# Kernel tuning notes

Hardware: AMD Instinct MI355X
Metric: run time of the kernel (lower is better)

## Reference

```python
import jax, jax.numpy as jnp
import numpy as np

B, C, H, W = 4, 256, 64, 64
R = 8          # rank = min(8, C//4)
G = 4          # conv groups
CG = C // G    # channels per group


def conv1x1(x, w, b):
    # x: [B,C,H,W], w: [O,C], b: [O]
    return jnp.einsum('oc,bchw->bohw', w, x) + b[None, :, None, None]


def conv1x1_grouped(x, w, b):
    # x: [B,C,H,W], w: [C, C//G] (per-output-channel slice of its group), b: [C]
    xg = x.reshape(B, G, CG, H, W)
    wg = w.reshape(G, CG, CG)  # [group, out_in_group, in_in_group]
    out = jnp.einsum('goc,bgchw->bgohw', wg, xg).reshape(B, C, H, W)
    return out + b[None, :, None, None]


def attend(q, k, v):
    # q,k: [B,R,H,W]; v: [B,C,H,W]; N = H*W
    qf = q.reshape(B, R, H * W)
    kf = k.reshape(B, R, H * W)
    vf = v.reshape(B, C, H * W)
    scores = jnp.einsum('bri,brj->bij', qf, kf)       # [B,N,N], no 1/sqrt scaling (faithful)
    attn = jax.nn.softmax(scores, axis=-1)
    out = jnp.einsum('bcm,bmn->bcn', vf, attn)        # v @ attn, contraction over query index m
    return out.reshape(B, C, H, W)


def setup_inputs():
    key = jax.random.key(0)
    ks = jax.random.split(key, 10)
    s = 0.05
    return {
        'fL': jax.random.normal(ks[0], (B, C, H, W), jnp.float32),
        'fU': jax.random.normal(ks[1], (B, C, H, W), jnp.float32),
        'qL_w': jax.random.normal(ks[2], (R, C), jnp.float32) * s,
        'qL_b': jnp.zeros((R,), jnp.float32),
        'kU_w': jax.random.normal(ks[3], (R, C), jnp.float32) * s,
        'kU_b': jnp.zeros((R,), jnp.float32),
        'vU_w': jax.random.normal(ks[4], (C, CG), jnp.float32) * s,
        'vU_b': jnp.zeros((C,), jnp.float32),
        'qU_w': jax.random.normal(ks[5], (R, C), jnp.float32) * s,
        'qU_b': jnp.zeros((R,), jnp.float32),
        'kL_w': jax.random.normal(ks[6], (R, C), jnp.float32) * s,
        'kL_b': jnp.zeros((R,), jnp.float32),
        'vL_w': jax.random.normal(ks[7], (C, CG), jnp.float32) * s,
        'vL_b': jnp.zeros((C,), jnp.float32),
        'beta': jnp.array(0.5, jnp.float32),
    }


def reference(fL, fU, qL_w, qL_b, kU_w, kU_b, vU_w, vU_b,
              qU_w, qU_b, kL_w, kL_b, vL_w, vL_b, beta):
    LU = attend(conv1x1(fL, qL_w, qL_b),
                conv1x1(fU, kU_w, kU_b),
                conv1x1_grouped(fU, vU_w, vU_b))
    UL = attend(conv1x1(fU, qU_w, qU_b),
                conv1x1(fL, kL_w, kL_b),
                conv1x1_grouped(fL, vL_w, vL_b))
    fL2 = fL + beta * LU
    fU2 = fU + beta * UL
    return (fL2, fU2)
```

## Files before the change

kernel.cpp:

```cpp
#include <hip/hip_runtime.h>

typedef float f32x4 __attribute__((ext_vector_type(4)));
typedef float f32x16 __attribute__((ext_vector_type(16)));
typedef short s16x8 __attribute__((ext_vector_type(8)));
typedef unsigned short u16;
typedef unsigned long long u64;

#define BN 4
#define CC 256
#define NN 4096

static __device__ __forceinline__ u16 f2bf(float x) {
    unsigned int u = __float_as_uint(x);
    u += 0x7FFF + ((u >> 16) & 1);
    return (u16)(u >> 16);
}

__global__ __launch_bounds__(256) void k_wtrans(
    const float* __restrict__ qLw, const float* __restrict__ kLw,
    const float* __restrict__ qUw, const float* __restrict__ kUw,
    const float* __restrict__ vUw, const float* __restrict__ vLw,
    float* __restrict__ wT, float* __restrict__ wvT)
{
    int a = blockIdx.x, t = threadIdx.x;
    const float* qw = a ? qUw : qLw;
    const float* kw = a ? kUw : kLw;
#pragma unroll
    for (int r = 0; r < 8; ++r) {
        wT[((size_t)a * 256 + t) * 16 + r]     = qw[r * 256 + t];
        wT[((size_t)a * 256 + t) * 16 + 8 + r] = kw[r * 256 + t];
    }
    const float* wv = a ? vLw : vUw;
    for (int cp = 0; cp < 64; ++cp)
        wvT[((size_t)a * 64 + cp) * 256 + t] = wv[(size_t)t * 64 + cp];
}

__global__ __launch_bounds__(256) void k_qkprep(
    const float* __restrict__ fL, const float* __restrict__ fU,
    const float* __restrict__ wT,
    const float* __restrict__ qLb, const float* __restrict__ kLb,
    const float* __restrict__ qUb, const float* __restrict__ kUb,
    u16* __restrict__ qbf, u16* __restrict__ kbf)
{
    int blk = blockIdx.x;
    int nc = blk & 31, b = (blk >> 5) & 3, src = blk >> 7;
    const float* f = src ? fU : fL;
    int qa = src, ka = 1 - src;
    int t = threadIdx.x;
    int nl = t & 127;
    int cs = __builtin_amdgcn_readfirstlane(t >> 7) * 128;
    int n = nc * 128 + nl;
    const float* fp = f + (size_t)b * 256 * NN + n;
    const float* wbase = wT + (size_t)src * 4096;

    float acc[16];
#pragma unroll
    for (int r = 0; r < 16; ++r) acc[r] = 0.f;

#pragma unroll 4
    for (int c = cs; c < cs + 128; ++c) {
        float fv = fp[(size_t)c * NN];
        const float* wr = wbase + (size_t)c * 16;
#pragma unroll
        for (int r = 0; r < 16; ++r) acc[r] += wr[r] * fv;
    }

    __shared__ float red[2][128][17];
    int cc = t >> 7;
#pragma unroll
    for (int r = 0; r < 16; ++r) red[cc][nl][r] = acc[r];
    __syncthreads();

    if (t < 128) {
        const float* bq = src ? qUb : qLb;
        const float* bk = src ? kUb : kLb;
        const float L2E = 1.4426950408889634f;
        int nn = nc * 128 + t;
        u16 pq[8], pk[8];
#pragma unroll
        for (int r = 0; r < 8; ++r) {
            pq[r] = f2bf((red[0][t][r]     + red[1][t][r]     + bq[r]) * L2E);
            pk[r] = f2bf( red[0][t][8 + r] + red[1][t][8 + r] + bk[r]);
        }
        uint4 vq, vk;
        vq.x = pq[0] | ((unsigned)pq[1] << 16); vq.y = pq[2] | ((unsigned)pq[3] << 16);
        vq.z = pq[4] | ((unsigned)pq[5] << 16); vq.w = pq[6] | ((unsigned)pq[7] << 16);
        vk.x = pk[0] | ((unsigned)pk[1] << 16); vk.y = pk[2] | ((unsigned)pk[3] << 16);
        vk.z = pk[4] | ((unsigned)pk[5] << 16); vk.w = pk[6] | ((unsigned)pk[7] << 16);
        *(uint4*)(qbf + (((size_t)qa * BN + b) * NN + nn) * 8) = vq;
        *(uint4*)(kbf + (((size_t)ka * BN + b) * NN + nn) * 8) = vk;
    }
}

__global__ __launch_bounds__(256) void k_zsum(
    const u16* __restrict__ qbf, const u16* __restrict__ kbf,
    float* __restrict__ Z)
{
    int blk = blockIdx.x;
    int mt = blk & 31, ab = blk >> 5;
    int t = threadIdx.x, l = t & 63;
    int w = __builtin_amdgcn_readfirstlane(t >> 6);
    int l31 = l & 31, g2 = l >> 5;
    int m0 = mt * 128 + w * 32;

    const u16* qab = qbf + (size_t)ab * NN * 8;
    const u16* kab = kbf + (size_t)ab * NN * 8;

    s16x8 af = *(const s16x8*)(qab + (size_t)(m0 + l31) * 8);
    if (g2) af = (s16x8)0;

    auto ldb = [&](int i) -> s16x8 {
        s16x8 r = *(const s16x8*)(kab + (size_t)(i * 32 + l31) * 8);
        return g2 ? (s16x8)0 : r;
    };

    float zp[16];
#pragma unroll
    for (int r = 0; r < 16; ++r) zp[r] = 0.f;

    s16x8 b0 = ldb(0), b1 = ldb(1);
#pragma unroll 1
    for (int i = 0; i < 128; ++i) {
        int nx = i + 2 < 127 ? i + 2 : 127;
        s16x8 bn = ldb(nx);
        f32x16 s = __builtin_amdgcn_mfma_f32_32x32x16_bf16(af, b0, (f32x16)0.f, 0, 0, 0);
#pragma unroll
        for (int r = 0; r < 16; ++r) zp[r] += __builtin_exp2f(s[r]);
        b0 = b1; b1 = bn;
    }

#pragma unroll
    for (int r = 0; r < 16; ++r) {
        float v = zp[r];
#pragma unroll
        for (int d = 1; d < 32; d <<= 1) v += __shfl_xor(v, d, 64);
        zp[r] = v;
    }
    if (l31 == 0) {
#pragma unroll
        for (int r = 0; r < 16; ++r) {
            int m = m0 + (r & 3) + 8 * (r >> 2) + 4 * g2;
            Z[(size_t)ab * NN + m] = zp[r];
        }
    }
}

__global__ __launch_bounds__(256) void k_vprep(
    const float* __restrict__ fL, const float* __restrict__ fU,
    const float* __restrict__ wvT,
    const float* __restrict__ vUb, const float* __restrict__ vLb,
    const float* __restrict__ Z, u16* __restrict__ vpt)
{
    int blk = blockIdx.x;
    int mc = blk & 31, g = (blk >> 5) & 3, ab = blk >> 7;
    int a = ab >> 2, b = ab & 3;
    const float* f    = a ? fL : fU;
    const float* bias = a ? vLb : vUb;
    int t = threadIdx.x, l = t & 63;
    int wu = __builtin_amdgcn_readfirstlane(t >> 6);
    int m0 = mc * 128 + l * 2;

    const float* fg = f + ((size_t)b * 256 + g * 64) * NN + m0;
    const float* wq = wvT + (size_t)a * 16384 + g * 64 + wu * 16;

    float acc[16][2];
#pragma unroll
    for (int j = 0; j < 16; ++j) { acc[j][0] = 0.f; acc[j][1] = 0.f; }

    for (int cp = 0; cp < 64; ++cp) {
        float2 fv = *(const float2*)(fg + (size_t)cp * NN);
        const float* wr = wq + (size_t)cp * 256;
        float4 w0 = *(const float4*)(wr);
        float4 w1 = *(const float4*)(wr + 4);
        float4 w2 = *(const float4*)(wr + 8);
        float4 w3 = *(const float4*)(wr + 12);
        float wv[16] = {w0.x,w0.y,w0.z,w0.w, w1.x,w1.y,w1.z,w1.w,
                        w2.x,w2.y,w2.z,w2.w, w3.x,w3.y,w3.z,w3.w};
#pragma unroll
        for (int j = 0; j < 16; ++j) {
            acc[j][0] += wv[j] * fv.x;
            acc[j][1] += wv[j] * fv.y;
        }
    }

    float2 z = *(const float2*)(Z + (size_t)ab * NN + m0);
    float zr0 = 1.f / z.x, zr1 = 1.f / z.y;
    int mt = m0 >> 5, mi = m0 & 31;
    u16* vpo = vpt + (((size_t)ab * 128 + mt) * 256 + g * 64 + wu * 16) * 32 + mi;
#pragma unroll
    for (int j = 0; j < 16; ++j) {
        float bj = bias[g * 64 + wu * 16 + j];
        unsigned pk = (unsigned)f2bf((acc[j][0] + bj) * zr0) |
                      ((unsigned)f2bf((acc[j][1] + bj) * zr1) << 16);
        *(unsigned*)(vpo + (size_t)j * 32) = pk;
    }
}

__global__ __launch_bounds__(512) void k_main(
    const float* __restrict__ fL, const float* __restrict__ fU,
    const u16* __restrict__ qbf, const u16* __restrict__ kbf,
    const u16* __restrict__ vpt, const float* __restrict__ beta_p,
    float* __restrict__ out)
{
    int blk = blockIdx.x;
    int ab = blk & 7, nt = blk >> 3;
    int a = ab >> 2, b = ab & 3;
    int n0 = nt * 128;
    int t = threadIdx.x, l = t & 63;
    int w = __builtin_amdgcn_readfirstlane(t >> 6);
    int c15 = l & 15, g = l >> 4;

    __shared__ u16 ebuf[2][128][40];

    const u16* qab = qbf + (size_t)ab * NN * 8;
    const u16* kab = kbf + (size_t)ab * NN * 8;

    s16x8 bkf = *(const s16x8*)(kab + (size_t)(n0 + w * 16 + c15) * 8);
    if (g) bkf = (s16x8)0;

    const u16* apb = vpt + (size_t)ab * (128ull * 8192)
                   + (size_t)(w * 32 + c15) * 32 + g * 8;

    f32x4 acc[2][8];
#pragma unroll
    for (int i = 0; i < 2; ++i)
#pragma unroll
        for (int j = 0; j < 8; ++j) acc[i][j] = (f32x4)0.f;

    auto qld = [&](int ks, int mh) -> s16x8 {
        s16x8 r = *(const s16x8*)(qab + (size_t)(ks * 32 + mh * 16 + c15) * 8);
        return g ? (s16x8)0 : r;
    };

    auto egen = [&](int pbuf, s16x8 qa0, s16x8 qa1) {
        f32x4 s0 = __builtin_amdgcn_mfma_f32_16x16x32_bf16(qa0, bkf, (f32x4)0.f, 0, 0, 0);
        f32x4 s1 = __builtin_amdgcn_mfma_f32_16x16x32_bf16(qa1, bkf, (f32x4)0.f, 0, 0, 0);
        u64 p0 = 0, p1 = 0;
#pragma unroll
        for (int r = 0; r < 4; ++r) {
            p0 |= (u64)f2bf(__builtin_exp2f(s0[r])) << (16 * r);
            p1 |= (u64)f2bf(__builtin_exp2f(s1[r])) << (16 * r);
        }
        *(u64*)&ebuf[pbuf][w * 16 + c15][4 * g]      = p0;
        *(u64*)&ebuf[pbuf][w * 16 + c15][16 + 4 * g] = p1;
    };

    auto pv = [&](int pbuf, const s16x8& a0, const s16x8& a1) {
#pragma unroll
        for (int nf = 0; nf < 8; ++nf) {
            s16x8 bf = *(const s16x8*)&ebuf[pbuf][nf * 16 + c15][8 * g];
            acc[0][nf] = __builtin_amdgcn_mfma_f32_16x16x32_bf16(a0, bf, acc[0][nf], 0, 0, 0);
            acc[1][nf] = __builtin_amdgcn_mfma_f32_16x16x32_bf16(a1, bf, acc[1][nf], 0, 0, 0);
        }
    };

    {
        s16x8 z0 = qld(0, 0), z1 = qld(0, 1);
        egen(0, z0, z1);
    }
    s16x8 qa0 = qld(1, 0), qa1 = qld(1, 1);
    s16x8 qb0 = qld(2, 0), qb1 = qld(2, 1);
    s16x8 af0 = *(const s16x8*)(apb);
    s16x8 af1 = *(const s16x8*)(apb + 512);
    __syncthreads();

#pragma unroll 1
    for (int k2 = 0; k2 < 64; ++k2) {
        {
            int k = 2 * k2;
            int kn = k + 1;
            const u16* apn = apb + (size_t)kn * 8192;
            s16x8 an0 = *(const s16x8*)(apn);
            s16x8 an1 = *(const s16x8*)(apn + 512);
            int kq = k + 3 < 127 ? k + 3 : 127;
            s16x8 nq0 = qld(kq, 0), nq1 = qld(kq, 1);

            egen(1, qa0, qa1);
            pv(0, af0, af1);

            af0 = an0; af1 = an1;
            qa0 = nq0; qa1 = nq1;
            __syncthreads();
        }
        {
            int k = 2 * k2 + 1;
            int kn = k + 1 < 127 ? k + 1 : 127;
            const u16* apn = apb + (size_t)kn * 8192;
            s16x8 an0 = *(const s16x8*)(apn);
            s16x8 an1 = *(const s16x8*)(apn + 512);
            int kq = k + 3 < 127 ? k + 3 : 127;
            s16x8 nq0 = qld(kq, 0), nq1 = qld(kq, 1);

            if (k < 127) egen(0, qb0, qb1);
            pv(1, af0, af1);

            af0 = an0; af1 = an1;
            qb0 = nq0; qb1 = nq1;
            __syncthreads();
        }
    }

    float beta = beta_p[0];
    const float* base = a ? fU : fL;
    float* op = out + (size_t)a * ((size_t)BN * CC * NN);
#pragma unroll
    for (int cf = 0; cf < 2; ++cf)
#pragma unroll
        for (int nf = 0; nf < 8; ++nf)
#pragma unroll
            for (int r = 0; r < 4; ++r) {
                int c = w * 32 + cf * 16 + g * 4 + r;
                int n = n0 + nf * 16 + c15;
                size_t idx = ((size_t)b * CC + c) * NN + n;
                op[idx] = base[idx] + beta * acc[cf][nf][r];
            }
}

extern "C" void kernel_launch(void* const* d_in, const int* in_sizes, int n_in,
                              void* d_out, int out_size, void* d_ws, size_t ws_size,
                              hipStream_t stream) {
    const float* fL  = (const float*)d_in[0];
    const float* fU  = (const float*)d_in[1];
    const float* qLw = (const float*)d_in[2];
    const float* qLb = (const float*)d_in[3];
    const float* kUw = (const float*)d_in[4];
    const float* kUb = (const float*)d_in[5];
    const float* vUw = (const float*)d_in[6];
    const float* vUb = (const float*)d_in[7];
    const float* qUw = (const float*)d_in[8];
    const float* qUb = (const float*)d_in[9];
    const float* kLw = (const float*)d_in[10];
    const float* kLb = (const float*)d_in[11];
    const float* vLw = (const float*)d_in[12];
    const float* vLb = (const float*)d_in[13];
    const float* beta = (const float*)d_in[14];

    char* ws = (char*)d_ws;
    float* wT  = (float*)(ws);
    float* wvT = (float*)(ws + 32768);
    u16*   qbf = (u16*)  (ws + 163840);
    u16*   kbf = (u16*)  (ws + 688128);
    float* Z   = (float*)(ws + 1212416);
    u16*   vpt = (u16*)  (ws + 1343488);
    float* out = (float*)d_out;

    k_wtrans<<<2, 256, 0, stream>>>(qLw, kLw, qUw, kUw, vUw, vLw, wT, wvT);
    k_qkprep<<<256, 256, 0, stream>>>(fL, fU, wT, qLb, kLb, qUb, kUb, qbf, kbf);
    k_zsum<<<256, 256, 0, stream>>>(qbf, kbf, Z);
    k_vprep<<<1024, 256, 0, stream>>>(fL, fU, wvT, vUb, vLb, Z, vpt);
    k_main<<<256, 512, 0, stream>>>(fL, fU, qbf, kbf, vpt, beta, out);
}
```

Measured before the change: 194.3 us.

## Retile attention PV loop to 64x64 warp tiles with swizzled LDS and deeper K step

The main attention kernel changes each warp's output tile from 32 channels x 128 positions to 64 channels x 64 positions. It processes 64 keys per iteration instead of 32, halving the number of barriers, and stores the exp tile in a 128-byte-row LDS buffer with an XOR swizzle to avoid bank conflicts. The new tiling cuts the LDS B-fragment reads per MFMA and rebalances reuse of V and exp fragments, at the cost of more registers for the 4x4 accumulators and the held fragments. Separately, the q/k projection kernel moves to 512 threads, splitting the channel reduction four ways for more parallelism.

After: 228.5 us. 1.18x slower.

```diff
diff --git a/kernel.cpp b/kernel.cpp
--- a/kernel.cpp
+++ b/kernel.cpp
@@ -35,7 +35,7 @@
         wvT[((size_t)a * 64 + cp) * 256 + t] = wv[(size_t)t * 64 + cp];
 }
 
-__global__ __launch_bounds__(256) void k_qkprep(
+__global__ __launch_bounds__(512) void k_qkprep(
     const float* __restrict__ fL, const float* __restrict__ fU,
     const float* __restrict__ wT,
     const float* __restrict__ qLb, const float* __restrict__ kLb,
@@ -48,7 +48,7 @@
     int qa = src, ka = 1 - src;
     int t = threadIdx.x;
     int nl = t & 127;
-    int cs = __builtin_amdgcn_readfirstlane(t >> 7) * 128;
+    int cs = __builtin_amdgcn_readfirstlane(t >> 7) * 64;
     int n = nc * 128 + nl;
     const float* fp = f + (size_t)b * 256 * NN + n;
     const float* wbase = wT + (size_t)src * 4096;
@@ -58,14 +58,14 @@
     for (int r = 0; r < 16; ++r) acc[r] = 0.f;
 
 #pragma unroll 4
-    for (int c = cs; c < cs + 128; ++c) {
+    for (int c = cs; c < cs + 64; ++c) {
         float fv = fp[(size_t)c * NN];
         const float* wr = wbase + (size_t)c * 16;
 #pragma unroll
         for (int r = 0; r < 16; ++r) acc[r] += wr[r] * fv;
     }
 
-    __shared__ float red[2][128][17];
+    __shared__ float red[4][128][17];
     int cc = t >> 7;
 #pragma unroll
     for (int r = 0; r < 16; ++r) red[cc][nl][r] = acc[r];
@@ -79,8 +79,10 @@
         u16 pq[8], pk[8];
 #pragma unroll
         for (int r = 0; r < 8; ++r) {
-            pq[r] = f2bf((red[0][t][r]     + red[1][t][r]     + bq[r]) * L2E);
-            pk[r] = f2bf( red[0][t][8 + r] + red[1][t][8 + r] + bk[r]);
+            float sq = red[0][t][r] + red[1][t][r] + red[2][t][r] + red[3][t][r];
+            float sk = red[0][t][8+r] + red[1][t][8+r] + red[2][t][8+r] + red[3][t][8+r];
+            pq[r] = f2bf((sq + bq[r]) * L2E);
+            pk[r] = f2bf( sk + bk[r]);
         }
         uint4 vq, vk;
         vq.x = pq[0] | ((unsigned)pq[1] << 16); vq.y = pq[2] | ((unsigned)pq[3] << 16);
@@ -209,8 +211,13 @@
     int t = threadIdx.x, l = t & 63;
     int w = __builtin_amdgcn_readfirstlane(t >> 6);
     int c15 = l & 15, g = l >> 4;
-
-    __shared__ u16 ebuf[2][128][40];
+    int cq = w & 3, nh = w >> 2;
+
+    __shared__ u16 ebuf[2][128][64];
+
+    auto eptr = [&](int p, int n, int mbyte) -> char* {
+        return ((char*)ebuf) + (((p << 7) + n) << 7) + (mbyte ^ ((n & 7) << 4));
+    };
 
     const u16* qab = qbf + (size_t)ab * NN * 8;
     const u16* kab = kbf + (size_t)ab * NN * 8;
@@ -219,98 +226,88 @@
     if (g) bkf = (s16x8)0;
 
     const u16* apb = vpt + (size_t)ab * (128ull * 8192)
-                   + (size_t)(w * 32 + c15) * 32 + g * 8;
-
-    f32x4 acc[2][8];
-#pragma unroll
-    for (int i = 0; i < 2; ++i)
-#pragma unroll
-        for (int j = 0; j < 8; ++j) acc[i][j] = (f32x4)0.f;
-
-    auto qld = [&](int ks, int mh) -> s16x8 {
-        s16x8 r = *(const s16x8*)(qab + (size_t)(ks * 32 + mh * 16 + c15) * 8);
+                   + (size_t)(cq * 64 + c15) * 32 + g * 8;
+
+    f32x4 acc[4][4];
+#pragma unroll
+    for (int i = 0; i < 4; ++i)
+#pragma unroll
+        for (int j = 0; j < 4; ++j) acc[i][j] = (f32x4)0.f;
+
+    auto qld = [&](int step, int mq) -> s16x8 {
+        s16x8 r = *(const s16x8*)(qab + (size_t)(step * 64 + mq * 16 + c15) * 8);
         return g ? (s16x8)0 : r;
     };
 
-    auto egen = [&](int pbuf, s16x8 qa0, s16x8 qa1) {
-        f32x4 s0 = __builtin_amdgcn_mfma_f32_16x16x32_bf16(qa0, bkf, (f32x4)0.f, 0, 0, 0);
-        f32x4 s1 = __builtin_amdgcn_mfma_f32_16x16x32_bf16(qa1, bkf, (f32x4)0.f, 0, 0, 0);
-        u64 p0 = 0, p1 = 0;
-#pragma unroll
-        for (int r = 0; r < 4; ++r) {
-            p0 |= (u64)f2bf(__builtin_exp2f(s0[r])) << (16 * r);
-            p1 |= (u64)f2bf(__builtin_exp2f(s1[r])) << (16 * r);
-        }
-        *(u64*)&ebuf[pbuf][w * 16 + c15][4 * g]      = p0;
-        *(u64*)&ebuf[pbuf][w * 16 + c15][16 + 4 * g] = p1;
+    auto egen = [&](int pbuf, const s16x8 (&qv)[4]) {
+#pragma unroll
+        for (int mq = 0; mq < 4; ++mq) {
+            f32x4 s = __builtin_amdgcn_mfma_f32_16x16x32_bf16(qv[mq], bkf, (f32x4)0.f, 0, 0, 0);
+            u64 pk = 0;
+#pragma unroll
+            for (int r = 0; r < 4; ++r)
+                pk |= (u64)f2bf(__builtin_exp2f(s[r])) << (16 * r);
+            *(u64*)eptr(pbuf, w * 16 + c15, mq * 32 + g * 8) = pk;
+        }
     };
 
-    auto pv = [&](int pbuf, const s16x8& a0, const s16x8& a1) {
-#pragma unroll
-        for (int nf = 0; nf < 8; ++nf) {
-            s16x8 bf = *(const s16x8*)&ebuf[pbuf][nf * 16 + c15][8 * g];
-            acc[0][nf] = __builtin_amdgcn_mfma_f32_16x16x32_bf16(a0, bf, acc[0][nf], 0, 0, 0);
-            acc[1][nf] = __builtin_amdgcn_mfma_f32_16x16x32_bf16(a1, bf, acc[1][nf], 0, 0, 0);
-        }
-    };
-
     {
-        s16x8 z0 = qld(0, 0), z1 = qld(0, 1);
-        egen(0, z0, z1);
-    }
-    s16x8 qa0 = qld(1, 0), qa1 = qld(1, 1);
-    s16x8 qb0 = qld(2, 0), qb1 = qld(2, 1);
-    s16x8 af0 = *(const s16x8*)(apb);
-    s16x8 af1 = *(const s16x8*)(apb + 512);
+        s16x8 q0[4];
+#pragma unroll
+        for (int mq = 0; mq < 4; ++mq) q0[mq] = qld(0, mq);
+        egen(0, q0);
+    }
+    s16x8 qn[4];
+#pragma unroll
+    for (int mq = 0; mq < 4; ++mq) qn[mq] = qld(1, mq);
     __syncthreads();
 
 #pragma unroll 1
-    for (int k2 = 0; k2 < 64; ++k2) {
-        {
-            int k = 2 * k2;
-            int kn = k + 1;
-            const u16* apn = apb + (size_t)kn * 8192;
-            s16x8 an0 = *(const s16x8*)(apn);
-            s16x8 an1 = *(const s16x8*)(apn + 512);
-            int kq = k + 3 < 127 ? k + 3 : 127;
-            s16x8 nq0 = qld(kq, 0), nq1 = qld(kq, 1);
-
-            egen(1, qa0, qa1);
-            pv(0, af0, af1);
-
-            af0 = an0; af1 = an1;
-            qa0 = nq0; qa1 = nq1;
-            __syncthreads();
-        }
-        {
-            int k = 2 * k2 + 1;
-            int kn = k + 1 < 127 ? k + 1 : 127;
-            const u16* apn = apb + (size_t)kn * 8192;
-            s16x8 an0 = *(const s16x8*)(apn);
-            s16x8 an1 = *(const s16x8*)(apn + 512);
-            int kq = k + 3 < 127 ? k + 3 : 127;
-            s16x8 nq0 = qld(kq, 0), nq1 = qld(kq, 1);
-
-            if (k < 127) egen(0, qb0, qb1);
-            pv(1, af0, af1);
-
-            af0 = an0; af1 = an1;
-            qb0 = nq0; qb1 = nq1;
-            __syncthreads();
-        }
+    for (int k = 0; k < 64; ++k) {
+        int p = k & 1;
+        const u16* at = apb + (size_t)(2 * k) * 8192;
+
+        s16x8 af[4][2];
+#pragma unroll
+        for (int cf = 0; cf < 4; ++cf) {
+            af[cf][0] = *(const s16x8*)(at + cf * 512);
+            af[cf][1] = *(const s16x8*)(at + 8192 + cf * 512);
+        }
+        s16x8 bf[4][2];
+#pragma unroll
+        for (int nf = 0; nf < 4; ++nf) {
+            bf[nf][0] = *(const s16x8*)eptr(p, nh * 64 + nf * 16 + c15, g * 16);
+            bf[nf][1] = *(const s16x8*)eptr(p, nh * 64 + nf * 16 + c15, 64 + g * 16);
+        }
+        if (k < 63) {
+            egen(p ^ 1, qn);
+            if (k < 62) {
+#pragma unroll
+                for (int mq = 0; mq < 4; ++mq) qn[mq] = qld(k + 2, mq);
+            }
+        }
+#pragma unroll
+        for (int kc = 0; kc < 2; ++kc)
+#pragma unroll
+            for (int cf = 0; cf < 4; ++cf)
+#pragma unroll
+                for (int nf = 0; nf < 4; ++nf)
+                    acc[cf][nf] = __builtin_amdgcn_mfma_f32_16x16x32_bf16(
+                        af[cf][kc], bf[nf][kc], acc[cf][nf], 0, 0, 0);
+        __syncthreads();
     }
 
     float beta = beta_p[0];
     const float* base = a ? fU : fL;
     float* op = out + (size_t)a * ((size_t)BN * CC * NN);
 #pragma unroll
-    for (int cf = 0; cf < 2; ++cf)
-#pragma unroll
-        for (int nf = 0; nf < 8; ++nf)
+    for (int cf = 0; cf < 4; ++cf)
+#pragma unroll
+        for (int nf = 0; nf < 4; ++nf)
 #pragma unroll
             for (int r = 0; r < 4; ++r) {
-                int c = w * 32 + cf * 16 + g * 4 + r;
-                int n = n0 + nf * 16 + c15;
+                int c = cq * 64 + cf * 16 + g * 4 + r;
+                int n = n0 + nh * 64 + nf * 16 + c15;
                 size_t idx = ((size_t)b * CC + c) * NN + n;
                 op[idx] = base[idx] + beta * acc[cf][nf][r];
             }
@@ -345,7 +342,7 @@
     float* out = (float*)d_out;
 
     k_wtrans<<<2, 256, 0, stream>>>(qLw, kLw, qUw, kUw, vUw, vLw, wT, wvT);
-    k_qkprep<<<256, 256, 0, stream>>>(fL, fU, wT, qLb, kLb, qUb, kUb, qbf, kbf);
+    k_qkprep<<<256, 512, 0, stream>>>(fL, fU, wT, qLb, kLb, qUb, kUb, qbf, kbf);
     k_zsum<<<256, 256, 0, stream>>>(qbf, kbf, Z);
     k_vprep<<<1024, 256, 0, stream>>>(fL, fU, wvT, vUb, vLb, Z, vpt);
     k_main<<<256, 512, 0, stream>>>(fL, fU, qbf, kbf, vpt, beta, out);
```
